# Kernel optimization log

Hardware: AMD Instinct MI355X
Metric: run time of the kernel (lower is better)

## Reference

```python
import jax, jax.numpy as jnp
import numpy as np

B, N, C = 64, 1024, 128
H1, H2 = 256, 128
ACTION = N


def _xavier(key, shape):
    lim = float(np.sqrt(6.0 / (shape[0] + shape[1])))
    return jax.random.uniform(key, shape, jnp.float32, -lim, lim)


def setup_inputs() -> dict:
    key = jax.random.key(0)
    ks = jax.random.split(key, 16)
    node_features = jax.random.normal(ks[0], (B, N, 3), jnp.float32)
    adjacency_matrix = jax.random.randint(ks[1], (B, N, N), 0, 2).astype(jnp.int32)
    return {
        "node_features": node_features,
        "adjacency_matrix": adjacency_matrix,
        "W_in": _xavier(ks[2], (3, C)),
        "a_src": _xavier(ks[3], (C, 1)),
        "a_dst": _xavier(ks[4], (C, 1)),
        "a_src2": _xavier(ks[5], (C, 1)),
        "a_dst2": _xavier(ks[6], (C, 1)),
        "W1": _xavier(ks[7], (C, H1)),
        "b1": jnp.zeros((H1,), jnp.float32),
        "W2": _xavier(ks[8], (H1, H2)),
        "b2": jnp.zeros((H2,), jnp.float32),
        "Wpi": _xavier(ks[9], (H2, ACTION)),
        "bpi": jnp.zeros((ACTION,), jnp.float32),
        "Wv": _xavier(ks[10], (H2, 1)),
        "bv": jnp.zeros((1,), jnp.float32),
    }


def _gat_layer(x, mask, a_src, a_dst):
    # x: [B,N,C]; mask: [B,N,N] bool
    ai = jnp.squeeze(x @ a_src, -1)  # [B,N] score of node as source (i)
    aj = jnp.squeeze(x @ a_dst, -1)  # [B,N] score of node as dest (j)
    e = ai[:, :, None] + aj[:, None, :]  # [B,N,N]
    e = jnp.where(e > 0, e, 0.2 * e)  # leaky_relu(0.2)
    e = jnp.where(mask, e, jnp.float32(-1e9))  # masked_fill(-inf)
    alpha = jax.nn.softmax(e, axis=-1)  # [B,N,N]
    out = jnp.einsum("bij,bjc->bic", alpha, x)  # weighted neighbor aggregation
    return jax.nn.relu(out)


def reference(node_features, adjacency_matrix, W_in, a_src, a_dst, a_src2, a_dst2,
              W1, b1, W2, b2, Wpi, bpi, Wv, bv):
    mask = adjacency_matrix > 0
    x = node_features @ W_in  # [B,N,C], no bias
    x = _gat_layer(x, mask, a_src, a_dst)
    x = _gat_layer(x, mask, a_src2, a_dst2)
    x = jnp.mean(x, axis=1)  # [B,C]
    x = jax.nn.relu(x @ W1 + b1)
    x = jax.nn.relu(x @ W2 + b2)
    pi = jax.nn.softmax(x @ Wpi + bpi, axis=1)
    v = x @ Wv + bv
    return (pi, v)
```

## Files before the change

### kernel.cpp

```cpp
#include <hip/hip_runtime.h>

#define Bn 64
#define Nn 1024
#define Cc 128

typedef _Float16 h8 __attribute__((ext_vector_type(8)));
typedef _Float16 h2v __attribute__((ext_vector_type(2)));
typedef float f4v __attribute__((ext_vector_type(4)));
typedef unsigned long long u64;

__global__ __launch_bounds__(256) void k_feat(
    const float* __restrict__ nf, const float* __restrict__ Win,
    const float* __restrict__ asrc, const float* __restrict__ adst,
    const int* __restrict__ adj, _Float16* __restrict__ X0, u64* __restrict__ pm,
    float* __restrict__ E, float* __restrict__ G,
    _Float16* __restrict__ Fh, _Float16* __restrict__ Hh) {
  int g = blockIdx.x; int b = g >> 7; int n0 = (g & 127) << 3;
  int t = threadIdx.x; int c = t >> 1; int h = t & 1;
  int lane = t & 63, wv = t >> 6;
  __shared__ float sNf[24];
  if (t < 24) sNf[t] = nf[((size_t)(b << 10) + n0) * 3 + t];
  float w0 = Win[c], w1 = Win[Cc + c], w2 = Win[2 * Cc + c];
  float as_ = asrc[c], ad = adst[c];
  __syncthreads();
  float ps[4], pd[4];
  _Float16 hv[4];
  #pragma unroll
  for (int r = 0; r < 4; r++) {
    const float* p = sNf + ((h << 2) + r) * 3;
    float x = p[0] * w0 + p[1] * w1 + p[2] * w2;
    hv[r] = (_Float16)x; ps[r] = x * as_; pd[r] = x * ad;
  }
  *(uint2*)(X0 + ((size_t)b << 17) + ((size_t)(g & 127) << 10) + (c << 3) + (h << 2)) = *(uint2*)hv;

  {
    ushort* pmu = (ushort*)pm;
    int row = n0 + (wv << 1);
    const uint4* ar = (const uint4*)(adj + (((size_t)(b << 10) + row) << 10));
    #pragma unroll
    for (int rr = 0; rr < 2; rr++) {
      uint4 v0 = ar[(lane << 2) | 0], v1 = ar[(lane << 2) | 1];
      uint4 v2 = ar[(lane << 2) | 2], v3 = ar[(lane << 2) | 3];
      unsigned int bits =
          (v0.x) | (v0.y << 1) | (v0.z << 2) | (v0.w << 3) |
          (v1.x << 4) | (v1.y << 5) | (v1.z << 6) | (v1.w << 7) |
          (v2.x << 8) | (v2.y << 9) | (v2.z << 10) | (v2.w << 11) |
          (v3.x << 12) | (v3.y << 13) | (v3.z << 14) | (v3.w << 15);
      pmu[(((size_t)(b << 10) + row + rr) << 6) + lane] = (ushort)bits;
      ar += 256;
    }
  }

  #pragma unroll
  for (int off = 32; off > 1; off >>= 1) {
    #pragma unroll
    for (int r = 0; r < 4; r++) { ps[r] += __shfl_down(ps[r], off, 64); pd[r] += __shfl_down(pd[r], off, 64); }
  }
  __shared__ float red[4][2][4][2];
  if (lane < 2) {
    #pragma unroll
    for (int r = 0; r < 4; r++) { red[wv][lane][r][0] = ps[r]; red[wv][lane][r][1] = pd[r]; }
  }
  __syncthreads();
  if (t < 8) {
    int hh = t >> 2, r = t & 3;
    float sa = 0.f, sd = 0.f;
    #pragma unroll
    for (int w = 0; w < 4; w++) { sa += red[w][hh][r][0]; sd += red[w][hh][r][1]; }
    int gi = (b << 10) + n0 + t;
    E[gi] = __expf(sa); G[gi] = __expf(0.2f * sa);
    Fh[gi] = (_Float16)__expf(sd); Hh[gi] = (_Float16)__expf(0.2f * sd);
  }
}

template <int LAYER>
__global__ __launch_bounds__(256, 3) void k_agg(
    const _Float16* __restrict__ X,
    const float* __restrict__ E, const float* __restrict__ G,
    const _Float16* __restrict__ Fh, const _Float16* __restrict__ Hh,
    const u64* __restrict__ pm, _Float16* __restrict__ Y, float* __restrict__ xmp,
    const float* __restrict__ as2, const float* __restrict__ ad2,
    float* __restrict__ E2o, float* __restrict__ G2o,
    _Float16* __restrict__ F2o, _Float16* __restrict__ H2o) {
  __shared__ __align__(16) char smem[34816];
  _Float16* s_Fh = (_Float16*)smem;
  _Float16* s_Hh = (_Float16*)(smem + 2048);
  unsigned char* s_pm = (unsigned char*)(smem + 4096);
  float* tile = (float*)smem;
  float* s_as2 = (float*)(smem + 33792);
  float* s_ad2 = (float*)(smem + 34304);

  const int lin = blockIdx.x;
  const int b = lin & 63, tile_id = lin >> 6, i0 = tile_id << 6;
  const int tid = threadIdx.x;
  const int lane = tid & 63, wv = tid >> 6;
  const int m = lane & 15, quad = lane >> 4;
  const int wi = wv >> 1, wc = wv & 1;
  const int gbase = b << 10;

  ((uint2*)s_Fh)[tid] = ((const uint2*)(Fh + gbase))[tid];
  ((uint2*)s_Hh)[tid] = ((const uint2*)(Hh + gbase))[tid];
  {
    const u64* pmg = pm + ((size_t)(gbase + i0) << 4);
    #pragma unroll
    for (int k = tid; k < 1024; k += 256) {
      int r = k >> 4, w = k & 15;
      *(u64*)(s_pm + r * 152 + (w << 3)) = pmg[k];
    }
  }
  if (LAYER == 1 && tid < 128) { s_as2[tid] = as2[tid]; s_ad2[tid] = ad2[tid]; }

  const int r0 = (wi << 5) + m;
  const int gi0 = gbase + i0 + r0;
  const _Float16 e0 = (_Float16)E[gi0],      g0 = (_Float16)G[gi0];
  const _Float16 e1 = (_Float16)E[gi0 + 16], g1 = (_Float16)G[gi0 + 16];
  const h2v E0p = {e0, e0}, G0p = {g0, g0}, E1p = {e1, e1}, G1p = {g1, g1};

  f4v acc[2][4];
  #pragma unroll
  for (int a = 0; a < 2; a++)
    #pragma unroll
    for (int ct = 0; ct < 4; ct++) { f4v z = {0.f, 0.f, 0.f, 0.f}; acc[a][ct] = z; }
  f4v accD0 = {0.f, 0.f, 0.f, 0.f}, accD1 = {0.f, 0.f, 0.f, 0.f};
  const h8 kOne = {(_Float16)1.f, (_Float16)1.f, (_Float16)1.f, (_Float16)1.f,
                   (_Float16)1.f, (_Float16)1.f, (_Float16)1.f, (_Float16)1.f};

  const char* gB = (const char*)(X + ((size_t)b << 17)) + (((quad << 7) + (wc << 6) + m) << 4);
  const unsigned char* pmr0 = s_pm + r0 * 152;
  const unsigned char* pmr1 = pmr0 + 16 * 152;

  __syncthreads();

  auto expand = [](unsigned mb, unsigned M[4]) {
    unsigned slo = ((mb & 0xFu) * 0x204081u) & 0x01010101u;
    unsigned shi = (((mb >> 4) & 0xFu) * 0x204081u) & 0x01010101u;
    slo *= 0xFFu; shi *= 0xFFu;
    M[0] = __builtin_amdgcn_perm(slo, slo, 0x01010000u);
    M[1] = __builtin_amdgcn_perm(slo, slo, 0x03030202u);
    M[2] = __builtin_amdgcn_perm(shi, shi, 0x01010000u);
    M[3] = __builtin_amdgcn_perm(shi, shi, 0x03030202u);
  };

  auto GL = [&](int kt, h8* Bf) {
    const char* gp = gB + ((size_t)kt << 13);
    Bf[0] = *(const h8*)gp;          Bf[1] = *(const h8*)(gp + 256);
    Bf[2] = *(const h8*)(gp + 512);  Bf[3] = *(const h8*)(gp + 768);
  };
  auto LL = [&](int kt, uint4& Fp, uint4& Hp, unsigned& mb0, unsigned& mb1) {
    const int j0 = (kt << 5) + (quad << 3);
    Fp = *(const uint4*)((const char*)s_Fh + (j0 << 1));
    Hp = *(const uint4*)((const char*)s_Hh + (j0 << 1));
    mb0 = pmr0[(kt << 2) + quad];    mb1 = pmr1[(kt << 2) + quad];
  };
  auto COMP = [&](const h8* Bf, uint4 Fp, uint4 Hp, unsigned mb0, unsigned mb1) {
    unsigned M0[4], M1[4];
    expand(mb0, M0); expand(mb1, M1);
    union { h8 v; unsigned u[4]; } A0, A1;
    const unsigned* fu = (const unsigned*)&Fp;
    const unsigned* hu = (const unsigned*)&Hp;
    #pragma unroll
    for (int q = 0; q < 4; q++) {
      h2v f2, h2;
      __builtin_memcpy(&f2, &fu[q], 4); __builtin_memcpy(&h2, &hu[q], 4);
      h2v mx0 = __builtin_elementwise_max(E0p * f2, G0p * h2);
      h2v mx1 = __builtin_elementwise_max(E1p * f2, G1p * h2);
      unsigned m0u, m1u;
      __builtin_memcpy(&m0u, &mx0, 4); __builtin_memcpy(&m1u, &mx1, 4);
      A0.u[q] = m0u & M0[q];
      A1.u[q] = m1u & M1[q];
    }
    __builtin_amdgcn_s_setprio(1);
    acc[0][0] = __builtin_amdgcn_mfma_f32_16x16x32_f16(A0.v, Bf[0], acc[0][0], 0, 0, 0);
    acc[1][0] = __builtin_amdgcn_mfma_f32_16x16x32_f16(A1.v, Bf[0], acc[1][0], 0, 0, 0);
    acc[0][1] = __builtin_amdgcn_mfma_f32_16x16x32_f16(A0.v, Bf[1], acc[0][1], 0, 0, 0);
    acc[1][1] = __builtin_amdgcn_mfma_f32_16x16x32_f16(A1.v, Bf[1], acc[1][1], 0, 0, 0);
    acc[0][2] = __builtin_amdgcn_mfma_f32_16x16x32_f16(A0.v, Bf[2], acc[0][2], 0, 0, 0);
    acc[1][2] = __builtin_amdgcn_mfma_f32_16x16x32_f16(A1.v, Bf[2], acc[1][2], 0, 0, 0);
    acc[0][3] = __builtin_amdgcn_mfma_f32_16x16x32_f16(A0.v, Bf[3], acc[0][3], 0, 0, 0);
    acc[1][3] = __builtin_amdgcn_mfma_f32_16x16x32_f16(A1.v, Bf[3], acc[1][3], 0, 0, 0);
    accD0 = __builtin_amdgcn_mfma_f32_16x16x32_f16(A0.v, kOne, accD0, 0, 0, 0);
    accD1 = __builtin_amdgcn_mfma_f32_16x16x32_f16(A1.v, kOne, accD1, 0, 0, 0);
    __builtin_amdgcn_s_setprio(0);
  };

  h8 B0[4], B1[4], B2[4], B3[4];
  uint4 Fp0, Hp0, Fp1, Hp1;
  unsigned ma0, mb0_, ma1, mb1_;
  GL(0, B0); GL(1, B1); LL(0, Fp0, Hp0, ma0, mb0_);
  for (int kt = 0; kt < 32; kt += 4) {
    GL(kt + 2, B2); LL(kt + 1, Fp1, Hp1, ma1, mb1_); COMP(B0, Fp0, Hp0, ma0, mb0_);
    GL(kt + 3, B3); LL(kt + 2, Fp0, Hp0, ma0, mb0_); COMP(B1, Fp1, Hp1, ma1, mb1_);
    GL(kt + 4, B0); LL(kt + 3, Fp1, Hp1, ma1, mb1_); COMP(B2, Fp0, Hp0, ma0, mb0_);
    GL(kt + 5, B1); LL(kt + 4, Fp0, Hp0, ma0, mb0_); COMP(B3, Fp1, Hp1, ma1, mb1_);
  }

  float rd8[2][4];
  #pragma unroll
  for (int r = 0; r < 4; r++) { rd8[0][r] = 1.0f / accD0[r]; rd8[1][r] = 1.0f / accD1[r]; }

  __syncthreads();
  #pragma unroll
  for (int a = 0; a < 2; a++)
    #pragma unroll
    for (int ct = 0; ct < 4; ct++)
      #pragma unroll
      for (int r = 0; r < 4; r++) {
        int lr = (wi << 5) + (a << 4) + (quad << 2) + r;
        int c = (wc << 6) + (ct << 4) + m;
        tile[lr * 132 + c] = fmaxf(acc[a][ct][r] * rd8[a][r], 0.f);
      }
  __syncthreads();
  if (LAYER == 1) {
    _Float16 hv[32];
    #pragma unroll
    for (int s = 0; s < 32; s++) {
      int q = (tid << 5) + s;
      int li = ((q >> 10) << 3) + (q & 7), c = (q >> 3) & 127;
      hv[s] = (_Float16)tile[li * 132 + c];
    }
    uint4* o = (uint4*)(Y + ((size_t)b << 17) + ((size_t)i0 << 7) + (tid << 5));
    o[0] = *(uint4*)&hv[0]; o[1] = *(uint4*)&hv[8];
    o[2] = *(uint4*)&hv[16]; o[3] = *(uint4*)&hv[24];
    {
      int i = tid >> 2, p = tid & 3, cb = p << 5;
      const float* trow = tile + i * 132 + cb;
      float ssrc = 0.f, sdst = 0.f;
      #pragma unroll
      for (int k = 0; k < 32; k += 4) {
        float4 tv = *(const float4*)(trow + k);
        float4 av = *(const float4*)(s_as2 + cb + k);
        float4 dv = *(const float4*)(s_ad2 + cb + k);
        ssrc += tv.x * av.x + tv.y * av.y + tv.z * av.z + tv.w * av.w;
        sdst += tv.x * dv.x + tv.y * dv.y + tv.z * dv.z + tv.w * dv.w;
      }
      ssrc += __shfl_xor(ssrc, 1, 64); ssrc += __shfl_xor(ssrc, 2, 64);
      sdst += __shfl_xor(sdst, 1, 64); sdst += __shfl_xor(sdst, 2, 64);
      int gi = gbase + i0 + i;
      if (p == 0) { E2o[gi] = __expf(ssrc); G2o[gi] = __expf(0.2f * ssrc); }
      else if (p == 1) { F2o[gi] = (_Float16)__expf(sdst); H2o[gi] = (_Float16)__expf(0.2f * sdst); }
    }
  } else {
    if (tid < 128) {
      float s = 0.f;
      #pragma unroll
      for (int i = 0; i < 64; i++) s += tile[i * 132 + tid];
      xmp[(((b << 4) + tile_id) << 7) + tid] = s;
    }
  }
}

__global__ __launch_bounds__(256) void k_head(
    const float* __restrict__ xmp, const float* __restrict__ W1, const float* __restrict__ b1,
    const float* __restrict__ W2, const float* __restrict__ b2,
    const float* __restrict__ Wpi, const float* __restrict__ bpi,
    const float* __restrict__ Wv, const float* __restrict__ bv,
    float* __restrict__ out) {
  int b = blockIdx.x, t = threadIdx.x;
  __shared__ float xs[128], h1[256], h2[128], red[4];
  if (t < 128) {
    const float* p = xmp + ((size_t)b << 11);
    float s = 0.f;
    #pragma unroll
    for (int xb = 0; xb < 16; xb++) s += p[(xb << 7) + t];
    xs[t] = s * (1.f / 1024.f);
  }
  __syncthreads();
  float s = 0.f;
  #pragma unroll 8
  for (int k = 0; k < 128; k++) s += xs[k] * W1[k * 256 + t];
  h1[t] = fmaxf(s + b1[t], 0.f);
  __syncthreads();
  if (t < 128) {
    float s2 = 0.f;
    #pragma unroll 8
    for (int k = 0; k < 256; k++) s2 += h1[k] * W2[k * 128 + t];
    h2[t] = fmaxf(s2 + b2[t], 0.f);
  }
  __syncthreads();
  float lg[4];
  #pragma unroll
  for (int q = 0; q < 4; q++) {
    int o = t + (q << 8);
    float s3 = 0.f;
    #pragma unroll 8
    for (int k = 0; k < 128; k++) s3 += h2[k] * Wpi[k * 1024 + o];
    lg[q] = s3 + bpi[o];
  }
  float mx = fmaxf(fmaxf(lg[0], lg[1]), fmaxf(lg[2], lg[3]));
  #pragma unroll
  for (int off = 32; off > 0; off >>= 1) mx = fmaxf(mx, __shfl_down(mx, off, 64));
  if ((t & 63) == 0) red[t >> 6] = mx;
  __syncthreads();
  mx = fmaxf(fmaxf(red[0], red[1]), fmaxf(red[2], red[3]));
  __syncthreads();
  float ex[4]; float sum = 0.f;
  #pragma unroll
  for (int q = 0; q < 4; q++) { ex[q] = __expf(lg[q] - mx); sum += ex[q]; }
  #pragma unroll
  for (int off = 32; off > 0; off >>= 1) sum += __shfl_down(sum, off, 64);
  if ((t & 63) == 0) red[t >> 6] = sum;
  __syncthreads();
  sum = red[0] + red[1] + red[2] + red[3];
  float rs = 1.0f / sum;
  #pragma unroll
  for (int q = 0; q < 4; q++) out[((size_t)b << 10) + t + (q << 8)] = ex[q] * rs;
  __syncthreads();
  float vp = (t < 128) ? h2[t] * Wv[t] : 0.f;
  #pragma unroll
  for (int off = 32; off > 0; off >>= 1) vp += __shfl_down(vp, off, 64);
  if ((t & 63) == 0) red[t >> 6] = vp;
  __syncthreads();
  if (t == 0) out[65536 + b] = red[0] + red[1] + red[2] + red[3] + bv[0];
}

extern "C" void kernel_launch(void* const* d_in, const int* in_sizes, int n_in,
                              void* d_out, int out_size, void* d_ws, size_t ws_size,
                              hipStream_t stream) {
  const float* nf    = (const float*)d_in[0];
  const int*   adj   = (const int*)  d_in[1];
  const float* Win   = (const float*)d_in[2];
  const float* asrc  = (const float*)d_in[3];
  const float* adst  = (const float*)d_in[4];
  const float* asrc2 = (const float*)d_in[5];
  const float* adst2 = (const float*)d_in[6];
  const float* W1    = (const float*)d_in[7];
  const float* b1    = (const float*)d_in[8];
  const float* W2    = (const float*)d_in[9];
  const float* b2    = (const float*)d_in[10];
  const float* Wpi   = (const float*)d_in[11];
  const float* bpi   = (const float*)d_in[12];
  const float* Wv    = (const float*)d_in[13];
  const float* bv    = (const float*)d_in[14];
  float* out = (float*)d_out;

  char* ws = (char*)d_ws;
  _Float16* x0 = (_Float16*)(ws);
  _Float16* x1 = (_Float16*)(ws + 16777216);
  u64* pm = (u64*)(ws + 33554432);
  char* S = ws + 41943040;
  float*    E1  = (float*)   (S + 2 * 262144);
  float*    G1  = (float*)   (S + 3 * 262144);
  _Float16* F1h = (_Float16*)(S + 4 * 262144);
  _Float16* H1h = (_Float16*)(S + 5 * 262144);
  float*    E2  = (float*)   (S + 8 * 262144);
  float*    G2  = (float*)   (S + 9 * 262144);
  _Float16* F2h = (_Float16*)(S + 10 * 262144);
  _Float16* H2h = (_Float16*)(S + 11 * 262144);
  float*    xmp = (float*)   (S + 12 * 262144);

  k_feat<<<8192, 256, 0, stream>>>(nf, Win, asrc, adst, adj, x0, pm, E1, G1, F1h, H1h);
  k_agg<1><<<1024, 256, 0, stream>>>(x0, E1, G1, F1h, H1h, pm, x1, nullptr,
                                     asrc2, adst2, E2, G2, F2h, H2h);
  k_agg<2><<<1024, 256, 0, stream>>>(x1, E2, G2, F2h, H2h, pm, nullptr, xmp,
                                     nullptr, nullptr, nullptr, nullptr, nullptr, nullptr);
  k_head<<<Bn, 256, 0, stream>>>(xmp, W1, b1, W2, b2, Wpi, bpi, Wv, bv, out);
}
```

Measured before the change: 501.3 us.

## Fuse MLP head into layer-2 aggregation via last-block atomic counter; two tiles per block

Removes the separate k_head launch. Layer-2 aggregation blocks now write partial column sums, bump a per-batch atomic counter, and the last block for each batch runs the MLP head and softmax. The counter is zeroed in k_feat. Each aggregation block also processes two 64-row tiles, which halves the grid to 512 blocks and reuses the Fh/Hh shared-memory loads across both tiles. The trade-off is fewer blocks (less parallelism on 256 CUs), more shared memory per block, and a serial head tail inside the last block of each batch.

```diff
diff --git a/kernel.cpp b/kernel.cpp
--- a/kernel.cpp
+++ b/kernel.cpp
@@ -14,10 +14,11 @@
     const float* __restrict__ asrc, const float* __restrict__ adst,
     const int* __restrict__ adj, _Float16* __restrict__ X0, u64* __restrict__ pm,
     float* __restrict__ E, float* __restrict__ G,
-    _Float16* __restrict__ Fh, _Float16* __restrict__ Hh) {
+    _Float16* __restrict__ Fh, _Float16* __restrict__ Hh, int* __restrict__ cnt) {
   int g = blockIdx.x; int b = g >> 7; int n0 = (g & 127) << 3;
   int t = threadIdx.x; int c = t >> 1; int h = t & 1;
   int lane = t & 63, wv = t >> 6;
+  if ((g & 127) == 0 && t == 0) cnt[b] = 0;
   __shared__ float sNf[24];
   if (t < 24) sNf[t] = nf[((size_t)(b << 10) + n0) * 3 + t];
   float w0 = Win[c], w1 = Win[Cc + c], w2 = Win[2 * Cc + c];
@@ -81,17 +82,27 @@
     const u64* __restrict__ pm, _Float16* __restrict__ Y, float* __restrict__ xmp,
     const float* __restrict__ as2, const float* __restrict__ ad2,
     float* __restrict__ E2o, float* __restrict__ G2o,
-    _Float16* __restrict__ F2o, _Float16* __restrict__ H2o) {
-  __shared__ __align__(16) char smem[34816];
+    _Float16* __restrict__ F2o, _Float16* __restrict__ H2o,
+    const float* __restrict__ W1, const float* __restrict__ b1,
+    const float* __restrict__ W2, const float* __restrict__ b2,
+    const float* __restrict__ Wpi, const float* __restrict__ bpi,
+    const float* __restrict__ Wv, const float* __restrict__ bv,
+    float* __restrict__ out, int* __restrict__ cnt) {
+  __shared__ __align__(16) char smem[48648];
   _Float16* s_Fh = (_Float16*)smem;
   _Float16* s_Hh = (_Float16*)(smem + 2048);
   unsigned char* s_pm = (unsigned char*)(smem + 4096);
-  float* tile = (float*)smem;
-  float* s_as2 = (float*)(smem + 33792);
-  float* s_ad2 = (float*)(smem + 34304);
+  float* tile = (float*)(smem + 13824);
+  float* s_as2 = (float*)(smem + 47616);
+  float* s_ad2 = (float*)(smem + 48128);
+  int* s_flag = (int*)(smem + 48640);
+  float* xs = (float*)smem;
+  float* h1 = (float*)(smem + 512);
+  float* h2 = (float*)(smem + 1536);
+  float* hred = (float*)(smem + 2048);
 
   const int lin = blockIdx.x;
-  const int b = lin & 63, tile_id = lin >> 6, i0 = tile_id << 6;
+  const int b = lin & 63, pair = lin >> 6;
   const int tid = threadIdx.x;
   const int lane = tid & 63, wv = tid >> 6;
   const int m = lane & 15, quad = lane >> 4;
@@ -100,36 +111,15 @@
 
   ((uint2*)s_Fh)[tid] = ((const uint2*)(Fh + gbase))[tid];
   ((uint2*)s_Hh)[tid] = ((const uint2*)(Hh + gbase))[tid];
-  {
-    const u64* pmg = pm + ((size_t)(gbase + i0) << 4);
-    #pragma unroll
-    for (int k = tid; k < 1024; k += 256) {
-      int r = k >> 4, w = k & 15;
-      *(u64*)(s_pm + r * 152 + (w << 3)) = pmg[k];
-    }
-  }
   if (LAYER == 1 && tid < 128) { s_as2[tid] = as2[tid]; s_ad2[tid] = ad2[tid]; }
 
   const int r0 = (wi << 5) + m;
-  const int gi0 = gbase + i0 + r0;
-  const _Float16 e0 = (_Float16)E[gi0],      g0 = (_Float16)G[gi0];
-  const _Float16 e1 = (_Float16)E[gi0 + 16], g1 = (_Float16)G[gi0 + 16];
-  const h2v E0p = {e0, e0}, G0p = {g0, g0}, E1p = {e1, e1}, G1p = {g1, g1};
-
-  f4v acc[2][4];
-  #pragma unroll
-  for (int a = 0; a < 2; a++)
-    #pragma unroll
-    for (int ct = 0; ct < 4; ct++) { f4v z = {0.f, 0.f, 0.f, 0.f}; acc[a][ct] = z; }
-  f4v accD0 = {0.f, 0.f, 0.f, 0.f}, accD1 = {0.f, 0.f, 0.f, 0.f};
+  const unsigned char* pmr0 = s_pm + r0 * 152;
+  const unsigned char* pmr1 = pmr0 + 16 * 152;
+  const char* gB = (const char*)(X + ((size_t)b << 17)) + (((quad << 7) + (wc << 6) + m) << 4);
+
   const h8 kOne = {(_Float16)1.f, (_Float16)1.f, (_Float16)1.f, (_Float16)1.f,
                    (_Float16)1.f, (_Float16)1.f, (_Float16)1.f, (_Float16)1.f};
-
-  const char* gB = (const char*)(X + ((size_t)b << 17)) + (((quad << 7) + (wc << 6) + m) << 4);
-  const unsigned char* pmr0 = s_pm + r0 * 152;
-  const unsigned char* pmr1 = pmr0 + 16 * 152;
-
-  __syncthreads();
 
   auto expand = [](unsigned mb, unsigned M[4]) {
     unsigned slo = ((mb & 0xFu) * 0x204081u) & 0x01010101u;
@@ -141,176 +131,205 @@
     M[3] = __builtin_amdgcn_perm(shi, shi, 0x03030202u);
   };
 
-  auto GL = [&](int kt, h8* Bf) {
-    const char* gp = gB + ((size_t)kt << 13);
-    Bf[0] = *(const h8*)gp;          Bf[1] = *(const h8*)(gp + 256);
-    Bf[2] = *(const h8*)(gp + 512);  Bf[3] = *(const h8*)(gp + 768);
-  };
-  auto LL = [&](int kt, uint4& Fp, uint4& Hp, unsigned& mb0, unsigned& mb1) {
-    const int j0 = (kt << 5) + (quad << 3);
-    Fp = *(const uint4*)((const char*)s_Fh + (j0 << 1));
-    Hp = *(const uint4*)((const char*)s_Hh + (j0 << 1));
-    mb0 = pmr0[(kt << 2) + quad];    mb1 = pmr1[(kt << 2) + quad];
-  };
-  auto COMP = [&](const h8* Bf, uint4 Fp, uint4 Hp, unsigned mb0, unsigned mb1) {
-    unsigned M0[4], M1[4];
-    expand(mb0, M0); expand(mb1, M1);
-    union { h8 v; unsigned u[4]; } A0, A1;
-    const unsigned* fu = (const unsigned*)&Fp;
-    const unsigned* hu = (const unsigned*)&Hp;
+  float colsum = 0.f;
+
+  #pragma unroll 1
+  for (int t2 = 0; t2 < 2; ++t2) {
+    const int i0 = (pair << 7) + (t2 << 6);
+    {
+      const u64* pmg = pm + ((size_t)(gbase + i0) << 4);
+      #pragma unroll
+      for (int k = tid; k < 1024; k += 256) {
+        int r = k >> 4, w = k & 15;
+        *(u64*)(s_pm + r * 152 + (w << 3)) = pmg[k];
+      }
+    }
+    __syncthreads();
+
+    const int gi0 = gbase + i0 + r0;
+    const _Float16 e0 = (_Float16)E[gi0],      g0 = (_Float16)G[gi0];
+    const _Float16 e1 = (_Float16)E[gi0 + 16], g1 = (_Float16)G[gi0 + 16];
+    const h2v E0p = {e0, e0}, G0p = {g0, g0}, E1p = {e1, e1}, G1p = {g1, g1};
+
+    f4v acc[2][4];
+    #pragma unroll
+    for (int a = 0; a < 2; a++)
+      #pragma unroll
+      for (int ct = 0; ct < 4; ct++) { f4v z = {0.f, 0.f, 0.f, 0.f}; acc[a][ct] = z; }
+    f4v accD0 = {0.f, 0.f, 0.f, 0.f}, accD1 = {0.f, 0.f, 0.f, 0.f};
+
+    auto GL = [&](int kt, h8* Bf) {
+      const char* gp = gB + ((size_t)kt << 13);
+      Bf[0] = *(const h8*)gp;          Bf[1] = *(const h8*)(gp + 256);
+      Bf[2] = *(const h8*)(gp + 512);  Bf[3] = *(const h8*)(gp + 768);
+    };
+    auto LL = [&](int kt, uint4& Fp, uint4& Hp, unsigned& mb0, unsigned& mb1) {
+      const int j0 = (kt << 5) + (quad << 3);
+      Fp = *(const uint4*)((const char*)s_Fh + (j0 << 1));
+      Hp = *(const uint4*)((const char*)s_Hh + (j0 << 1));
+      mb0 = pmr0[(kt << 2) + quad];    mb1 = pmr1[(kt << 2) + quad];
+    };
+    auto COMP = [&](const h8* Bf, uint4 Fp, uint4 Hp, unsigned mb0, unsigned mb1) {
+      unsigned M0[4], M1[4];
+      expand(mb0, M0); expand(mb1, M1);
+      union { h8 v; unsigned u[4]; } A0, A1;
+      const unsigned* fu = (const unsigned*)&Fp;
+      const unsigned* hu = (const unsigned*)&Hp;
+      #pragma unroll
+      for (int q = 0; q < 4; q++) {
+        h2v f2, h2;
+        __builtin_memcpy(&f2, &fu[q], 4); __builtin_memcpy(&h2, &hu[q], 4);
+        h2v mx0 = __builtin_elementwise_max(E0p * f2, G0p * h2);
+        h2v mx1 = __builtin_elementwise_max(E1p * f2, G1p * h2);
+        unsigned m0u, m1u;
+        __builtin_memcpy(&m0u, &mx0, 4); __builtin_memcpy(&m1u, &mx1, 4);
+        A0.u[q] = m0u & M0[q];
+        A1.u[q] = m1u & M1[q];
+      }
+      __builtin_amdgcn_s_setprio(1);
+      acc[0][0] = __builtin_amdgcn_mfma_f32_16x16x32_f16(A0.v, Bf[0], acc[0][0], 0, 0, 0);
+      acc[1][0] = __builtin_amdgcn_mfma_f32_16x16x32_f16(A1.v, Bf[0], acc[1][0], 0, 0, 0);
+      acc[0][1] = __builtin_amdgcn_mfma_f32_16x16x32_f16(A0.v, Bf[1], acc[0][1], 0, 0, 0);
+      acc[1][1] = __builtin_amdgcn_mfma_f32_16x16x32_f16(A1.v, Bf[1], acc[1][1], 0, 0, 0);
+      acc[0][2] = __builtin_amdgcn_mfma_f32_16x16x32_f16(A0.v, Bf[2], acc[0][2], 0, 0, 0);
+      acc[1][2] = __builtin_amdgcn_mfma_f32_16x16x32_f16(A1.v, Bf[2], acc[1][2], 0, 0, 0);
+      acc[0][3] = __builtin_amdgcn_mfma_f32_16x16x32_f16(A0.v, Bf[3], acc[0][3], 0, 0, 0);
+      acc[1][3] = __builtin_amdgcn_mfma_f32_16x16x32_f16(A1.v, Bf[3], acc[1][3], 0, 0, 0);
+      accD0 = __builtin_amdgcn_mfma_f32_16x16x32_f16(A0.v, kOne, accD0, 0, 0, 0);
+      accD1 = __builtin_amdgcn_mfma_f32_16x16x32_f16(A1.v, kOne, accD1, 0, 0, 0);
+      __builtin_amdgcn_s_setprio(0);
+    };
+
+    h8 B0[4], B1[4], B2[4], B3[4];
+    uint4 Fp0, Hp0, Fp1, Hp1;
+    unsigned ma0, mb0_, ma1, mb1_;
+    GL(0, B0); GL(1, B1); LL(0, Fp0, Hp0, ma0, mb0_);
+    for (int kt = 0; kt < 32; kt += 4) {
+      GL(kt + 2, B2); LL(kt + 1, Fp1, Hp1, ma1, mb1_); COMP(B0, Fp0, Hp0, ma0, mb0_);
+      GL(kt + 3, B3); LL(kt + 2, Fp0, Hp0, ma0, mb0_); COMP(B1, Fp1, Hp1, ma1, mb1_);
+      GL(kt + 4, B0); LL(kt + 3, Fp1, Hp1, ma1, mb1_); COMP(B2, Fp0, Hp0, ma0, mb0_);
+      GL(kt + 5, B1); LL(kt + 4, Fp0, Hp0, ma0, mb0_); COMP(B3, Fp1, Hp1, ma1, mb1_);
+    }
+
+    float rd8[2][4];
+    #pragma unroll
+    for (int r = 0; r < 4; r++) { rd8[0][r] = 1.0f / accD0[r]; rd8[1][r] = 1.0f / accD1[r]; }
+
+    #pragma unroll
+    for (int a = 0; a < 2; a++)
+      #pragma unroll
+      for (int ct = 0; ct < 4; ct++)
+        #pragma unroll
+        for (int r = 0; r < 4; r++) {
+          int lr = (wi << 5) + (a << 4) + (quad << 2) + r;
+          int c = (wc << 6) + (ct << 4) + m;
+          tile[lr * 132 + c] = fmaxf(acc[a][ct][r] * rd8[a][r], 0.f);
+        }
+    __syncthreads();
+
+    if (LAYER == 1) {
+      _Float16 hv[32];
+      #pragma unroll
+      for (int s = 0; s < 32; s++) {
+        int q = (tid << 5) + s;
+        int li = ((q >> 10) << 3) + (q & 7), c = (q >> 3) & 127;
+        hv[s] = (_Float16)tile[li * 132 + c];
+      }
+      uint4* o = (uint4*)(Y + ((size_t)b << 17) + ((size_t)i0 << 7) + (tid << 5));
+      o[0] = *(uint4*)&hv[0]; o[1] = *(uint4*)&hv[8];
+      o[2] = *(uint4*)&hv[16]; o[3] = *(uint4*)&hv[24];
+      {
+        int i = tid >> 2, p = tid & 3, cb = p << 5;
+        const float* trow = tile + i * 132 + cb;
+        float ssrc = 0.f, sdst = 0.f;
+        #pragma unroll
+        for (int k = 0; k < 32; k += 4) {
+          float4 tv = *(const float4*)(trow + k);
+          float4 av = *(const float4*)(s_as2 + cb + k);
+          float4 dv = *(const float4*)(s_ad2 + cb + k);
+          ssrc += tv.x * av.x + tv.y * av.y + tv.z * av.z + tv.w * av.w;
+          sdst += tv.x * dv.x + tv.y * dv.y + tv.z * dv.z + tv.w * dv.w;
+        }
+        ssrc += __shfl_xor(ssrc, 1, 64); ssrc += __shfl_xor(ssrc, 2, 64);
+        sdst += __shfl_xor(sdst, 1, 64); sdst += __shfl_xor(sdst, 2, 64);
+        int gi = gbase + i0 + i;
+        if (p == 0) { E2o[gi] = __expf(ssrc); G2o[gi] = __expf(0.2f * ssrc); }
+        else if (p == 1) { F2o[gi] = (_Float16)__expf(sdst); H2o[gi] = (_Float16)__expf(0.2f * sdst); }
+      }
+    } else {
+      if (tid < 128) {
+        float s = 0.f;
+        #pragma unroll
+        for (int i = 0; i < 64; i++) s += tile[i * 132 + tid];
+        colsum += s;
+      }
+    }
+  }
+
+  if (LAYER == 2) {
+    if (tid < 128) xmp[(((b << 3) + pair) << 7) + tid] = colsum;
+    __threadfence();
+    __syncthreads();
+    if (tid == 0) s_flag[0] = atomicAdd(&cnt[b], 1);
+    __syncthreads();
+    if (s_flag[0] != 7) return;
+    __threadfence();
+    const int t = tid;
+    if (t < 128) {
+      const float* p = xmp + ((size_t)b << 10);
+      float s = 0.f;
+      #pragma unroll
+      for (int xb = 0; xb < 8; xb++) s += p[(xb << 7) + t];
+      xs[t] = s * (1.f / 1024.f);
+    }
+    __syncthreads();
+    float s = 0.f;
+    #pragma unroll 8
+    for (int k = 0; k < 128; k++) s += xs[k] * W1[k * 256 + t];
+    h1[t] = fmaxf(s + b1[t], 0.f);
+    __syncthreads();
+    if (t < 128) {
+      float s2 = 0.f;
+      #pragma unroll 8
+      for (int k = 0; k < 256; k++) s2 += h1[k] * W2[k * 128 + t];
+      h2[t] = fmaxf(s2 + b2[t], 0.f);
+    }
+    __syncthreads();
+    float lg[4];
     #pragma unroll
     for (int q = 0; q < 4; q++) {
-      h2v f2, h2;
-      __builtin_memcpy(&f2, &fu[q], 4); __builtin_memcpy(&h2, &hu[q], 4);
-      h2v mx0 = __builtin_elementwise_max(E0p * f2, G0p * h2);
-      h2v mx1 = __builtin_elementwise_max(E1p * f2, G1p * h2);
-      unsigned m0u, m1u;
-      __builtin_memcpy(&m0u, &mx0, 4); __builtin_memcpy(&m1u, &mx1, 4);
-      A0.u[q] = m0u & M0[q];
-      A1.u[q] = m1u & M1[q];
-    }
-    __builtin_amdgcn_s_setprio(1);
-    acc[0][0] = __builtin_amdgcn_mfma_f32_16x16x32_f16(A0.v, Bf[0], acc[0][0], 0, 0, 0);
-    acc[1][0] = __builtin_amdgcn_mfma_f32_16x16x32_f16(A1.v, Bf[0], acc[1][0], 0, 0, 0);
-    acc[0][1] = __builtin_amdgcn_mfma_f32_16x16x32_f16(A0.v, Bf[1], acc[0][1], 0, 0, 0);
-    acc[1][1] = __builtin_amdgcn_mfma_f32_16x16x32_f16(A1.v, Bf[1], acc[1][1], 0, 0, 0);
-    acc[0][2] = __builtin_amdgcn_mfma_f32_16x16x32_f16(A0.v, Bf[2], acc[0][2], 0, 0, 0);
-    acc[1][2] = __builtin_amdgcn_mfma_f32_16x16x32_f16(A1.v, Bf[2], acc[1][2], 0, 0, 0);
-    acc[0][3] = __builtin_amdgcn_mfma_f32_16x16x32_f16(A0.v, Bf[3], acc[0][3], 0, 0, 0);
-    acc[1][3] = __builtin_amdgcn_mfma_f32_16x16x32_f16(A1.v, Bf[3], acc[1][3], 0, 0, 0);
-    accD0 = __builtin_amdgcn_mfma_f32_16x16x32_f16(A0.v, kOne, accD0, 0, 0, 0);
-    accD1 = __builtin_amdgcn_mfma_f32_16x16x32_f16(A1.v, kOne, accD1, 0, 0, 0);
-    __builtin_amdgcn_s_setprio(0);
-  };
-
-  h8 B0[4], B1[4], B2[4], B3[4];
-  uint4 Fp0, Hp0, Fp1, Hp1;
-  unsigned ma0, mb0_, ma1, mb1_;
-  GL(0, B0); GL(1, B1); LL(0, Fp0, Hp0, ma0, mb0_);
-  for (int kt = 0; kt < 32; kt += 4) {
-    GL(kt + 2, B2); LL(kt + 1, Fp1, Hp1, ma1, mb1_); COMP(B0, Fp0, Hp0, ma0, mb0_);
-    GL(kt + 3, B3); LL(kt + 2, Fp0, Hp0, ma0, mb0_); COMP(B1, Fp1, Hp1, ma1, mb1_);
-    GL(kt + 4, B0); LL(kt + 3, Fp1, Hp1, ma1, mb1_); COMP(B2, Fp0, Hp0, ma0, mb0_);
-    GL(kt + 5, B1); LL(kt + 4, Fp0, Hp0, ma0, mb0_); COMP(B3, Fp1, Hp1, ma1, mb1_);
-  }
-
-  float rd8[2][4];
-  #pragma unroll
-  for (int r = 0; r < 4; r++) { rd8[0][r] = 1.0f / accD0[r]; rd8[1][r] = 1.0f / accD1[r]; }
-
-  __syncthreads();
-  #pragma unroll
-  for (int a = 0; a < 2; a++)
-    #pragma unroll
-    for (int ct = 0; ct < 4; ct++)
-      #pragma unroll
-      for (int r = 0; r < 4; r++) {
-        int lr = (wi << 5) + (a << 4) + (quad << 2) + r;
-        int c = (wc << 6) + (ct << 4) + m;
-        tile[lr * 132 + c] = fmaxf(acc[a][ct][r] * rd8[a][r], 0.f);
-      }
-  __syncthreads();
-  if (LAYER == 1) {
-    _Float16 hv[32];
-    #pragma unroll
-    for (int s = 0; s < 32; s++) {
-      int q = (tid << 5) + s;
-      int li = ((q >> 10) << 3) + (q & 7), c = (q >> 3) & 127;
-      hv[s] = (_Float16)tile[li * 132 + c];
-    }
-    uint4* o = (uint4*)(Y + ((size_t)b << 17) + ((size_t)i0 << 7) + (tid << 5));
-    o[0] = *(uint4*)&hv[0]; o[1] = *(uint4*)&hv[8];
-    o[2] = *(uint4*)&hv[16]; o[3] = *(uint4*)&hv[24];
-    {
-      int i = tid >> 2, p = tid & 3, cb = p << 5;
-      const float* trow = tile + i * 132 + cb;
-      float ssrc = 0.f, sdst = 0.f;
-      #pragma unroll
-      for (int k = 0; k < 32; k += 4) {
-        float4 tv = *(const float4*)(trow + k);
-        float4 av = *(const float4*)(s_as2 + cb + k);
-        float4 dv = *(const float4*)(s_ad2 + cb + k);
-        ssrc += tv.x * av.x + tv.y * av.y + tv.z * av.z + tv.w * av.w;
-        sdst += tv.x * dv.x + tv.y * dv.y + tv.z * dv.z + tv.w * dv.w;
-      }
-      ssrc += __shfl_xor(ssrc, 1, 64); ssrc += __shfl_xor(ssrc, 2, 64);
-      sdst += __shfl_xor(sdst, 1, 64); sdst += __shfl_xor(sdst, 2, 64);
-      int gi = gbase + i0 + i;
-      if (p == 0) { E2o[gi] = __expf(ssrc); G2o[gi] = __expf(0.2f * ssrc); }
-      else if (p == 1) { F2o[gi] = (_Float16)__expf(sdst); H2o[gi] = (_Float16)__expf(0.2f * sdst); }
-    }
-  } else {
-    if (tid < 128) {
-      float s = 0.f;
-      #pragma unroll
-      for (int i = 0; i < 64; i++) s += tile[i * 132 + tid];
-      xmp[(((b << 4) + tile_id) << 7) + tid] = s;
-    }
-  }
-}
-
-__global__ __launch_bounds__(256) void k_head(
-    const float* __restrict__ xmp, const float* __restrict__ W1, const float* __restrict__ b1,
-    const float* __restrict__ W2, const float* __restrict__ b2,
-    const float* __restrict__ Wpi, const float* __restrict__ bpi,
-    const float* __restrict__ Wv, const float* __restrict__ bv,
-    float* __restrict__ out) {
-  int b = blockIdx.x, t = threadIdx.x;
-  __shared__ float xs[128], h1[256], h2[128], red[4];
-  if (t < 128) {
-    const float* p = xmp + ((size_t)b << 11);
-    float s = 0.f;
-    #pragma unroll
-    for (int xb = 0; xb < 16; xb++) s += p[(xb << 7) + t];
-    xs[t] = s * (1.f / 1024.f);
-  }
-  __syncthreads();
-  float s = 0.f;
-  #pragma unroll 8
-  for (int k = 0; k < 128; k++) s += xs[k] * W1[k * 256 + t];
-  h1[t] = fmaxf(s + b1[t], 0.f);
-  __syncthreads();
-  if (t < 128) {
-    float s2 = 0.f;
-    #pragma unroll 8
-    for (int k = 0; k < 256; k++) s2 += h1[k] * W2[k * 128 + t];
-    h2[t] = fmaxf(s2 + b2[t], 0.f);
-  }
-  __syncthreads();
-  float lg[4];
-  #pragma unroll
-  for (int q = 0; q < 4; q++) {
-    int o = t + (q << 8);
-    float s3 = 0.f;
-    #pragma unroll 8
-    for (int k = 0; k < 128; k++) s3 += h2[k] * Wpi[k * 1024 + o];
-    lg[q] = s3 + bpi[o];
-  }
-  float mx = fmaxf(fmaxf(lg[0], lg[1]), fmaxf(lg[2], lg[3]));
-  #pragma unroll
-  for (int off = 32; off > 0; off >>= 1) mx = fmaxf(mx, __shfl_down(mx, off, 64));
-  if ((t & 63) == 0) red[t >> 6] = mx;
-  __syncthreads();
-  mx = fmaxf(fmaxf(red[0], red[1]), fmaxf(red[2], red[3]));
-  __syncthreads();
-  float ex[4]; float sum = 0.f;
-  #pragma unroll
-  for (int q = 0; q < 4; q++) { ex[q] = __expf(lg[q] - mx); sum += ex[q]; }
-  #pragma unroll
-  for (int off = 32; off > 0; off >>= 1) sum += __shfl_down(sum, off, 64);
-  if ((t & 63) == 0) red[t >> 6] = sum;
-  __syncthreads();
-  sum = red[0] + red[1] + red[2] + red[3];
-  float rs = 1.0f / sum;
-  #pragma unroll
-  for (int q = 0; q < 4; q++) out[((size_t)b << 10) + t + (q << 8)] = ex[q] * rs;
-  __syncthreads();
-  float vp = (t < 128) ? h2[t] * Wv[t] : 0.f;
-  #pragma unroll
-  for (int off = 32; off > 0; off >>= 1) vp += __shfl_down(vp, off, 64);
-  if ((t & 63) == 0) red[t >> 6] = vp;
-  __syncthreads();
-  if (t == 0) out[65536 + b] = red[0] + red[1] + red[2] + red[3] + bv[0];
+      int o = t + (q << 8);
+      float s3 = 0.f;
+      #pragma unroll 8
+      for (int k = 0; k < 128; k++) s3 += h2[k] * Wpi[k * 1024 + o];
+      lg[q] = s3 + bpi[o];
+    }
+    float mx = fmaxf(fmaxf(lg[0], lg[1]), fmaxf(lg[2], lg[3]));
+    #pragma unroll
+    for (int off = 32; off > 0; off >>= 1) mx = fmaxf(mx, __shfl_down(mx, off, 64));
+    if ((t & 63) == 0) hred[t >> 6] = mx;
+    __syncthreads();
+    mx = fmaxf(fmaxf(hred[0], hred[1]), fmaxf(hred[2], hred[3]));
+    __syncthreads();
+    float ex[4]; float sum = 0.f;
+    #pragma unroll
+    for (int q = 0; q < 4; q++) { ex[q] = __expf(lg[q] - mx); sum += ex[q]; }
+    #pragma unroll
+    for (int off = 32; off > 0; off >>= 1) sum += __shfl_down(sum, off, 64);
+    if ((t & 63) == 0) hred[t >> 6] = sum;
+    __syncthreads();
+    sum = hred[0] + hred[1] + hred[2] + hred[3];
+    float rs = 1.0f / sum;
+    #pragma unroll
+    for (int q = 0; q < 4; q++) out[((size_t)b << 10) + t + (q << 8)] = ex[q] * rs;
+    __syncthreads();
+    float vp = (t < 128) ? h2[t] * Wv[t] : 0.f;
+    #pragma unroll
+    for (int off = 32; off > 0; off >>= 1) vp += __shfl_down(vp, off, 64);
+    if ((t & 63) == 0) hred[t >> 6] = vp;
+    __syncthreads();
+    if (t == 0) out[65536 + b] = hred[0] + hred[1] + hred[2] + hred[3] + bv[0];
+  }
 }
 
 extern "C" void kernel_launch(void* const* d_in, const int* in_sizes, int n_in,
@@ -347,11 +366,14 @@
   _Float16* F2h = (_Float16*)(S + 10 * 262144);
   _Float16* H2h = (_Float16*)(S + 11 * 262144);
   float*    xmp = (float*)   (S + 12 * 262144);
-
-  k_feat<<<8192, 256, 0, stream>>>(nf, Win, asrc, adst, adj, x0, pm, E1, G1, F1h, H1h);
-  k_agg<1><<<1024, 256, 0, stream>>>(x0, E1, G1, F1h, H1h, pm, x1, nullptr,
-                                     asrc2, adst2, E2, G2, F2h, H2h);
-  k_agg<2><<<1024, 256, 0, stream>>>(x1, E2, G2, F2h, H2h, pm, nullptr, xmp,
-                                     nullptr, nullptr, nullptr, nullptr, nullptr, nullptr);
-  k_head<<<Bn, 256, 0, stream>>>(xmp, W1, b1, W2, b2, Wpi, bpi, Wv, bv, out);
+  int*      cnt = (int*)     (S + 13 * 262144);
+
+  k_feat<<<8192, 256, 0, stream>>>(nf, Win, asrc, adst, adj, x0, pm, E1, G1, F1h, H1h, cnt);
+  k_agg<1><<<512, 256, 0, stream>>>(x0, E1, G1, F1h, H1h, pm, x1, nullptr,
+                                    asrc2, adst2, E2, G2, F2h, H2h,
+                                    nullptr, nullptr, nullptr, nullptr,
+                                    nullptr, nullptr, nullptr, nullptr, nullptr, nullptr);
+  k_agg<2><<<512, 256, 0, stream>>>(x1, E2, G2, F2h, H2h, pm, nullptr, xmp,
+                                    nullptr, nullptr, nullptr, nullptr, nullptr, nullptr,
+                                    W1, b1, W2, b2, Wpi, bpi, Wv, bv, out, cnt);
 }
```

Result: slower. 540.1 us (+7.7%).
